# Optimization experiments

Measured on AMD Instinct MI355X. Metric: run time of the kernel, lower is better.

Reference implementation:

```python
import jax, jax.numpy as jnp
import numpy as np

IN_FEATURES = 4096
OUT_FEATURES = 4096
R = 16

def setup_inputs() -> dict:
    key = jax.random.key(0)
    k1, k2 = jax.random.split(key)
    x = jax.random.normal(k1, (4, 2048, IN_FEATURES), dtype=jnp.float32)
    # Original init: B = zeros, A = randn. Use randn for B too so the output
    # is non-trivial for correctness testing (math is identical regardless).
    lora_matrix_B = jax.random.normal(k2, (OUT_FEATURES, R), dtype=jnp.float32) * 0.02
    lora_matrix_A = jax.random.normal(jax.random.fold_in(key, 1), (R, IN_FEATURES), dtype=jnp.float32)
    return {"x": x, "lora_matrix_B": lora_matrix_B, "lora_matrix_A": lora_matrix_A}

def reference(x, lora_matrix_B, lora_matrix_A):
    # lora_weights = B @ A  -> [out_features, in_features]
    lora_weights = jnp.matmul(lora_matrix_B, lora_matrix_A)
    # F.linear(x, W) = x @ W^T
    return jnp.einsum('bsi,oi->bso', x, lora_weights)
```

## Files before the change

### kernel.cpp

```cpp
#include <hip/hip_runtime.h>

#define K_DIM   4096
#define N_DIM   4096
#define M_ROWS  8192
#define KF      (K_DIM / 4)
#define NF      (N_DIM / 4)
#define KSPLIT  8
#define KCH     (KF / KSPLIT)
#define NTILES  (M_ROWS / 16)
#define TP_F4_STRIDE (M_ROWS * 16 / 4)

__global__ __launch_bounds__(256, 4) void lora_xat(const float* __restrict__ x,
                                                   const float* __restrict__ A,
                                                   float* __restrict__ tpart) {
    __shared__ float4 Alds[16 * KCH];

    const int tid  = threadIdx.x;
    const int wv   = tid >> 6;
    const int lane = tid & 63;
    const int rb   = blockIdx.x >> 3;
    const int h    = blockIdx.x & 7;
    const int row0 = rb * 16 + wv * 4;
    const int kbase = h * KCH;

    const float4* x4 = (const float4*)x;
    const float4* A4 = (const float4*)A;

    #pragma unroll
    for (int i = 0; i < 8; ++i) {
        const int idx = i * 256 + tid;
        const int r = idx >> 7;
        const int c = idx & (KCH - 1);
        Alds[idx] = A4[r * KF + kbase + c];
    }

    float red[64];
    #pragma unroll
    for (int v = 0; v < 64; ++v) red[v] = 0.f;

    __syncthreads();

    #pragma unroll
    for (int it = 0; it < 2; ++it) {
        const int kl = it * 64 + lane;
        const int kf = kbase + kl;
        float4 xv[4];
        #pragma unroll
        for (int j = 0; j < 4; ++j)
            xv[j] = x4[(size_t)(row0 + j) * KF + kf];
        #pragma unroll
        for (int r = 0; r < 16; ++r) {
            const float4 av = Alds[r * KCH + kl];
            #pragma unroll
            for (int j = 0; j < 4; ++j) {
                float a = red[j * 16 + r];
                a = fmaf(xv[j].x, av.x, a);
                a = fmaf(xv[j].y, av.y, a);
                a = fmaf(xv[j].z, av.z, a);
                a = fmaf(xv[j].w, av.w, a);
                red[j * 16 + r] = a;
            }
        }
    }

    #pragma unroll
    for (int s = 0; s < 6; ++s) {
        const int m = 1 << s;
        const int b = (lane >> s) & 1;
        #pragma unroll
        for (int u = 0; u < (64 >> (s + 1)); ++u) {
            const float lo = red[2 * u];
            const float hi = red[2 * u + 1];
            const float send = b ? lo : hi;
            const float recv = __shfl_xor(send, m, 64);
            const float kept = b ? hi : lo;
            red[u] = kept + recv;
        }
    }

    tpart[((size_t)h * M_ROWS + row0) * 16 + lane] = red[0];
}

__global__ __launch_bounds__(256, 4) void lora_tb(const float* __restrict__ tpart,
                                                  const float* __restrict__ B,
                                                  float* __restrict__ out) {
    __shared__ float4 tp_s[4][64];
    __shared__ float4 t_s4[64];

    const int tid = threadIdx.x;
    const int rb  = blockIdx.x >> 2;
    const int cb  = blockIdx.x & 3;

    const int o0 = cb * 1024 + tid * 4;
    float4 breg[4][4];
    const float4* B4 = (const float4*)B;
    #pragma unroll
    for (int j = 0; j < 4; ++j)
        #pragma unroll
        for (int q = 0; q < 4; ++q)
            breg[j][q] = B4[(size_t)(o0 + j) * 4 + q];

    {
        const int f  = tid & 63;
        const int hp = tid >> 6;
        const float4* p4 = (const float4*)tpart;
        float4 a = p4[(size_t)(2 * hp) * TP_F4_STRIDE + rb * 64 + f];
        const float4 b = p4[(size_t)(2 * hp + 1) * TP_F4_STRIDE + rb * 64 + f];
        a.x += b.x; a.y += b.y; a.z += b.z; a.w += b.w;
        tp_s[hp][f] = a;
    }
    __syncthreads();
    if (tid < 64) {
        float4 s = tp_s[0][tid];
        #pragma unroll
        for (int hp = 1; hp < 4; ++hp) {
            const float4 q = tp_s[hp][tid];
            s.x += q.x; s.y += q.y; s.z += q.z; s.w += q.w;
        }
        t_s4[tid] = s;
    }
    __syncthreads();

    float4* out4 = (float4*)out;
    const int c4 = cb * 256 + tid;

    #pragma unroll
    for (int row = 0; row < 16; ++row) {
        float4 tq[4];
        #pragma unroll
        for (int q = 0; q < 4; ++q)
            tq[q] = t_s4[row * 4 + q];
        float o0v = 0.f, o1v = 0.f, o2v = 0.f, o3v = 0.f;
        #pragma unroll
        for (int r = 0; r < 16; ++r) {
            const float4 tv4 = tq[r >> 2];
            const float tv = ((r & 3) == 0) ? tv4.x :
                             ((r & 3) == 1) ? tv4.y :
                             ((r & 3) == 2) ? tv4.z : tv4.w;
            o0v = fmaf(tv, ((const float*)&breg[0][0])[r], o0v);
            o1v = fmaf(tv, ((const float*)&breg[1][0])[r], o1v);
            o2v = fmaf(tv, ((const float*)&breg[2][0])[r], o2v);
            o3v = fmaf(tv, ((const float*)&breg[3][0])[r], o3v);
        }
        const float4 o = {o0v, o1v, o2v, o3v};
        out4[(size_t)(rb * 16 + row) * NF + c4] = o;
    }
}

extern "C" void kernel_launch(void* const* d_in, const int* in_sizes, int n_in,
                              void* d_out, int out_size, void* d_ws, size_t ws_size,
                              hipStream_t stream) {
    const float* x = (const float*)d_in[0];
    const float* B = (const float*)d_in[1];
    const float* A = (const float*)d_in[2];
    float* out = (float*)d_out;

    float* tpart = (float*)d_ws;

    lora_xat<<<NTILES * KSPLIT, 256, 0, stream>>>(x, A, tpart);
    lora_tb<<<NTILES * (N_DIM / 1024), 256, 0, stream>>>(tpart, B, out);
}
```

Baseline: 66.07 us.

## Reduce K-split to two and software-pipeline A/x chunk loads through registers

The first kernel now splits K into 2 halves instead of 8. Each block loops over 4 chunks of 128 float4s, double-buffering the next chunk's A and x loads in registers while computing the current one from LDS. This cuts the partial-sum writes and the second kernel's reduction from 8 partials to 2, which simplifies lora_tb. The cost is fewer blocks (1024 instead of 4096) and more registers per thread (launch bounds lowered to 2), so there is less parallelism for hiding memory latency on a bandwidth-bound read of x.

```diff
diff --git a/kernel.cpp b/kernel.cpp
--- a/kernel.cpp
+++ b/kernel.cpp
@@ -5,12 +5,14 @@
 #define M_ROWS  8192
 #define KF      (K_DIM / 4)
 #define NF      (N_DIM / 4)
-#define KSPLIT  8
-#define KCH     (KF / KSPLIT)
+#define KSPLIT  2
+#define KHALF   (KF / KSPLIT)
+#define KCH     128
+#define NCH     (KHALF / KCH)
 #define NTILES  (M_ROWS / 16)
 #define TP_F4_STRIDE (M_ROWS * 16 / 4)
 
-__global__ __launch_bounds__(256, 4) void lora_xat(const float* __restrict__ x,
+__global__ __launch_bounds__(256, 2) void lora_xat(const float* __restrict__ x,
                                                    const float* __restrict__ A,
                                                    float* __restrict__ tpart) {
     __shared__ float4 Alds[16 * KCH];
@@ -18,47 +20,82 @@
     const int tid  = threadIdx.x;
     const int wv   = tid >> 6;
     const int lane = tid & 63;
-    const int rb   = blockIdx.x >> 3;
-    const int h    = blockIdx.x & 7;
+    const int rb   = blockIdx.x >> 1;
+    const int h    = blockIdx.x & 1;
     const int row0 = rb * 16 + wv * 4;
-    const int kbase = h * KCH;
+    const int kbase = h * KHALF;
 
     const float4* x4 = (const float4*)x;
     const float4* A4 = (const float4*)A;
+
+    const int st_r[8] = {0,0,0,0,0,0,0,0}; (void)st_r;
+
+    float4 areg[8];
+    float4 xreg[2][8];
 
     #pragma unroll
     for (int i = 0; i < 8; ++i) {
         const int idx = i * 256 + tid;
         const int r = idx >> 7;
         const int c = idx & (KCH - 1);
-        Alds[idx] = A4[r * KF + kbase + c];
+        areg[i] = A4[r * KF + kbase + c];
     }
+    #pragma unroll
+    for (int it = 0; it < 2; ++it)
+        #pragma unroll
+        for (int j = 0; j < 4; ++j)
+            xreg[0][it * 4 + j] =
+                x4[(size_t)(row0 + j) * KF + kbase + it * 64 + lane];
 
     float red[64];
     #pragma unroll
     for (int v = 0; v < 64; ++v) red[v] = 0.f;
 
-    __syncthreads();
+    #pragma unroll
+    for (int ch = 0; ch < NCH; ++ch) {
+        const int cur = ch & 1;
+        const int nxt = cur ^ 1;
 
-    #pragma unroll
-    for (int it = 0; it < 2; ++it) {
-        const int kl = it * 64 + lane;
-        const int kf = kbase + kl;
-        float4 xv[4];
+        __syncthreads();
         #pragma unroll
-        for (int j = 0; j < 4; ++j)
-            xv[j] = x4[(size_t)(row0 + j) * KF + kf];
+        for (int i = 0; i < 8; ++i) {
+            const int idx = i * 256 + tid;
+            Alds[idx] = areg[i];
+        }
+        if (ch + 1 < NCH) {
+            const int kc = kbase + (ch + 1) * KCH;
+            #pragma unroll
+            for (int i = 0; i < 8; ++i) {
+                const int idx = i * 256 + tid;
+                const int r = idx >> 7;
+                const int c = idx & (KCH - 1);
+                areg[i] = A4[r * KF + kc + c];
+            }
+            #pragma unroll
+            for (int it = 0; it < 2; ++it)
+                #pragma unroll
+                for (int j = 0; j < 4; ++j)
+                    xreg[nxt][it * 4 + j] =
+                        x4[(size_t)(row0 + j) * KF + kc + it * 64 + lane];
+        }
+        __syncthreads();
+
         #pragma unroll
-        for (int r = 0; r < 16; ++r) {
-            const float4 av = Alds[r * KCH + kl];
+        for (int it = 0; it < 2; ++it) {
+            const int kl = it * 64 + lane;
             #pragma unroll
-            for (int j = 0; j < 4; ++j) {
-                float a = red[j * 16 + r];
-                a = fmaf(xv[j].x, av.x, a);
-                a = fmaf(xv[j].y, av.y, a);
-                a = fmaf(xv[j].z, av.z, a);
-                a = fmaf(xv[j].w, av.w, a);
-                red[j * 16 + r] = a;
+            for (int r = 0; r < 16; ++r) {
+                const float4 av = Alds[r * KCH + kl];
+                #pragma unroll
+                for (int j = 0; j < 4; ++j) {
+                    float a = red[j * 16 + r];
+                    const float4 xv = xreg[cur][it * 4 + j];
+                    a = fmaf(xv.x, av.x, a);
+                    a = fmaf(xv.y, av.y, a);
+                    a = fmaf(xv.z, av.z, a);
+                    a = fmaf(xv.w, av.w, a);
+                    red[j * 16 + r] = a;
+                }
             }
         }
     }
@@ -84,7 +121,6 @@
 __global__ __launch_bounds__(256, 4) void lora_tb(const float* __restrict__ tpart,
                                                   const float* __restrict__ B,
                                                   float* __restrict__ out) {
-    __shared__ float4 tp_s[4][64];
     __shared__ float4 t_s4[64];
 
     const int tid = threadIdx.x;
@@ -100,24 +136,12 @@
         for (int q = 0; q < 4; ++q)
             breg[j][q] = B4[(size_t)(o0 + j) * 4 + q];
 
-    {
-        const int f  = tid & 63;
-        const int hp = tid >> 6;
+    if (tid < 64) {
         const float4* p4 = (const float4*)tpart;
-        float4 a = p4[(size_t)(2 * hp) * TP_F4_STRIDE + rb * 64 + f];
-        const float4 b = p4[(size_t)(2 * hp + 1) * TP_F4_STRIDE + rb * 64 + f];
+        float4 a = p4[(size_t)rb * 64 + tid];
+        const float4 b = p4[(size_t)TP_F4_STRIDE + rb * 64 + tid];
         a.x += b.x; a.y += b.y; a.z += b.z; a.w += b.w;
-        tp_s[hp][f] = a;
-    }
-    __syncthreads();
-    if (tid < 64) {
-        float4 s = tp_s[0][tid];
-        #pragma unroll
-        for (int hp = 1; hp < 4; ++hp) {
-            const float4 q = tp_s[hp][tid];
-            s.x += q.x; s.y += q.y; s.z += q.z; s.w += q.w;
-        }
-        t_s4[tid] = s;
+        t_s4[tid] = a;
     }
     __syncthreads();
 
```

Measured after the change: 107.7 us. +63.1%, slower.

## Compute x@A^T with bf16 MFMA instead of scalar FMA and shuffle reduction

Applied to the files above, without the earlier changes.

The first-stage kernel now converts x and A to bf16 in registers and accumulates x@A^T with 16x16x32 bf16 MFMA instructions, replacing the FP32 FMA loops, the LDS staging of A and the long cross-lane shuffle reduction. Each block now covers 64 rows and a wave handles 16 rows, with A read directly from global memory. This targets the ALU and shuffle cost of the stage that reads x, so it becomes closer to memory-bound. In exchange it lowers precision to bf16 inputs, which may strain the correctness tolerance, and it reads A uncached from global instead of LDS.

```diff
diff --git a/kernel.cpp b/kernel.cpp
--- a/kernel.cpp
+++ b/kernel.cpp
@@ -6,79 +6,64 @@
 #define KF      (K_DIM / 4)
 #define NF      (N_DIM / 4)
 #define KSPLIT  8
-#define KCH     (KF / KSPLIT)
 #define NTILES  (M_ROWS / 16)
 #define TP_F4_STRIDE (M_ROWS * 16 / 4)
 
-__global__ __launch_bounds__(256, 4) void lora_xat(const float* __restrict__ x,
-                                                   const float* __restrict__ A,
-                                                   float* __restrict__ tpart) {
-    __shared__ float4 Alds[16 * KCH];
+typedef __attribute__((ext_vector_type(8))) short short8v;
+typedef __attribute__((ext_vector_type(4))) float f32x4;
 
+static __device__ __forceinline__ short f2bf(float f) {
+    const unsigned u = __builtin_bit_cast(unsigned, f);
+    return (short)((u + 0x7FFFu + ((u >> 16) & 1u)) >> 16);
+}
+
+__global__ __launch_bounds__(256) void lora_xat(const float* __restrict__ x,
+                                                const float* __restrict__ A,
+                                                float* __restrict__ tpart) {
     const int tid  = threadIdx.x;
     const int wv   = tid >> 6;
     const int lane = tid & 63;
     const int rb   = blockIdx.x >> 3;
     const int h    = blockIdx.x & 7;
-    const int row0 = rb * 16 + wv * 4;
-    const int kbase = h * KCH;
+    const int row0 = rb * 64 + wv * 16;
+
+    const int mrow = row0 + (lane & 15);
+    const int acol = lane & 15;
+    const int og   = (lane >> 4) * 2;
 
     const float4* x4 = (const float4*)x;
     const float4* A4 = (const float4*)A;
+    const size_t xbase = (size_t)mrow * KF;
+    const size_t abase = (size_t)acol * KF;
 
-    #pragma unroll
-    for (int i = 0; i < 8; ++i) {
-        const int idx = i * 256 + tid;
-        const int r = idx >> 7;
-        const int c = idx & (KCH - 1);
-        Alds[idx] = A4[r * KF + kbase + c];
-    }
+    f32x4 acc = {0.f, 0.f, 0.f, 0.f};
 
-    float red[64];
-    #pragma unroll
-    for (int v = 0; v < 64; ++v) red[v] = 0.f;
+    #pragma unroll 4
+    for (int it = 0; it < 16; ++it) {
+        const int kf = h * 128 + it * 8 + og;
+        const float4 xa = x4[xbase + kf];
+        const float4 xb = x4[xbase + kf + 1];
+        const float4 aa = A4[abase + kf];
+        const float4 ab = A4[abase + kf + 1];
 
-    __syncthreads();
+        short8v af, bf;
+        af[0] = f2bf(xa.x); af[1] = f2bf(xa.y);
+        af[2] = f2bf(xa.z); af[3] = f2bf(xa.w);
+        af[4] = f2bf(xb.x); af[5] = f2bf(xb.y);
+        af[6] = f2bf(xb.z); af[7] = f2bf(xb.w);
+        bf[0] = f2bf(aa.x); bf[1] = f2bf(aa.y);
+        bf[2] = f2bf(aa.z); bf[3] = f2bf(aa.w);
+        bf[4] = f2bf(ab.x); bf[5] = f2bf(ab.y);
+        bf[6] = f2bf(ab.z); bf[7] = f2bf(ab.w);
 
-    #pragma unroll
-    for (int it = 0; it < 2; ++it) {
-        const int kl = it * 64 + lane;
-        const int kf = kbase + kl;
-        float4 xv[4];
-        #pragma unroll
-        for (int j = 0; j < 4; ++j)
-            xv[j] = x4[(size_t)(row0 + j) * KF + kf];
-        #pragma unroll
-        for (int r = 0; r < 16; ++r) {
-            const float4 av = Alds[r * KCH + kl];
-            #pragma unroll
-            for (int j = 0; j < 4; ++j) {
-                float a = red[j * 16 + r];
-                a = fmaf(xv[j].x, av.x, a);
-                a = fmaf(xv[j].y, av.y, a);
-                a = fmaf(xv[j].z, av.z, a);
-                a = fmaf(xv[j].w, av.w, a);
-                red[j * 16 + r] = a;
-            }
-        }
+        acc = __builtin_amdgcn_mfma_f32_16x16x32_bf16(af, bf, acc, 0, 0, 0);
     }
 
     #pragma unroll
-    for (int s = 0; s < 6; ++s) {
-        const int m = 1 << s;
-        const int b = (lane >> s) & 1;
-        #pragma unroll
-        for (int u = 0; u < (64 >> (s + 1)); ++u) {
-            const float lo = red[2 * u];
-            const float hi = red[2 * u + 1];
-            const float send = b ? lo : hi;
-            const float recv = __shfl_xor(send, m, 64);
-            const float kept = b ? hi : lo;
-            red[u] = kept + recv;
-        }
+    for (int v = 0; v < 4; ++v) {
+        const int orow = row0 + (lane >> 4) * 4 + v;
+        tpart[((size_t)h * M_ROWS + orow) * 16 + (lane & 15)] = acc[v];
     }
-
-    tpart[((size_t)h * M_ROWS + row0) * 16 + lane] = red[0];
 }
 
 __global__ __launch_bounds__(256, 4) void lora_tb(const float* __restrict__ tpart,
@@ -157,6 +142,6 @@
 
     float* tpart = (float*)d_ws;
 
-    lora_xat<<<NTILES * KSPLIT, 256, 0, stream>>>(x, A, tpart);
+    lora_xat<<<(M_ROWS / 64) * KSPLIT, 256, 0, stream>>>(x, A, tpart);
     lora_tb<<<NTILES * (N_DIM / 1024), 256, 0, stream>>>(tpart, B, out);
 }
```

Result: no change. 65.71 us (-0.5%).
